# Optimization experiments

Hardware: AMD Instinct MI355X
Metric: run time of the kernel (lower is better)

## Reference

```python
import jax, jax.numpy as jnp
import numpy as np

LN_EPS = 1e-5


def setup_inputs() -> dict:
    key = jax.random.key(0)
    ks = jax.random.split(key, 6)
    B, M, N, D = 16, 128, 128, 128
    NM, H = 16, 512
    xav = float(np.sqrt(2.0 / (D + D)))  # xavier_normal over (in_dim, out_dim) fan
    return {
        "x": jax.random.normal(ks[0], (B, M, N, D), jnp.float32),
        "w1": jax.random.normal(ks[1], (D, D, NM, 2), jnp.float32) * xav,
        "w2": jax.random.normal(ks[2], (D, D, NM, 2), jnp.float32) * xav,
        "ff_w0": jax.random.normal(ks[3], (D, H), jnp.float32) * float(1.0 / np.sqrt(D)),
        "ff_b0": jnp.zeros((H,), jnp.float32),
        "ff_w1": jax.random.normal(ks[4], (H, D), jnp.float32) * float(1.0 / np.sqrt(H)),
        "ff_b1": jnp.zeros((D,), jnp.float32),
        "ln_g": jnp.ones((D,), jnp.float32),
        "ln_b": jnp.zeros((D,), jnp.float32),
    }


def _layer_norm(h, g, b):
    mu = jnp.mean(h, axis=-1, keepdims=True)
    var = jnp.mean(jnp.square(h - mu), axis=-1, keepdims=True)
    return (h - mu) * jax.lax.rsqrt(var + LN_EPS) * g + b


def _forward_fourier(x, w1, w2):
    # x: [B, M, N, I] -> [B, I, M, N]
    xt = jnp.transpose(x, (0, 3, 1, 2))
    B, I, M, N = xt.shape
    nm = w1.shape[2]
    cw1 = w1[..., 0] + 1j * w1[..., 1]  # [I, O, nm]
    cw2 = w2[..., 0] + 1j * w2[..., 1]
    O = cw1.shape[1]

    # Fourier along last axis (y)
    fty = jnp.fft.rfft(xt, axis=-1, norm="ortho")                    # [B,I,M,N//2+1]
    f1 = jnp.einsum("bixy,ioy->boxy", fty[..., :nm], cw1)            # [B,O,M,nm]
    pad_y = jnp.zeros((B, O, M, N // 2 + 1 - nm), dtype=f1.dtype)
    xy = jnp.fft.irfft(jnp.concatenate([f1, pad_y], axis=-1), n=N, axis=-1, norm="ortho")

    # Fourier along second-to-last axis (x)
    ftx = jnp.fft.rfft(xt, axis=-2, norm="ortho")                    # [B,I,M//2+1,N]
    f2 = jnp.einsum("bixy,iox->boxy", ftx[:, :, :nm, :], cw2)        # [B,O,nm,N]
    pad_x = jnp.zeros((B, O, M // 2 + 1 - nm, N), dtype=f2.dtype)
    xx = jnp.fft.irfft(jnp.concatenate([f2, pad_x], axis=-2), n=M, axis=-2, norm="ortho")

    return jnp.transpose(xx + xy, (0, 2, 3, 1))  # [B,M,N,O]


def reference(x, w1, w2, ff_w0, ff_b0, ff_w1, ff_b1, ln_g, ln_b):
    h = _forward_fourier(x, w1, w2)
    # backcast FeedForward: Linear -> ReLU -> Linear -> LayerNorm (dropout=0)
    h1 = jax.nn.relu(jnp.einsum("bmni,ih->bmnh", h, ff_w0) + ff_b0)
    h2 = jnp.einsum("bmnh,ho->bmno", h1, ff_w1) + ff_b1
    return _layer_norm(h2, ln_g, ln_b)
```

## Files before the change

kernel.cpp:

```cpp
#include <hip/hip_runtime.h>


#define LN_EPS 1e-5f
#define NMODES 16
#define FROW 4096
#define HROW 16384

typedef __attribute__((ext_vector_type(8))) short short8;
typedef __attribute__((ext_vector_type(8))) ushort ushort8;
typedef __attribute__((ext_vector_type(4))) short short4v;
typedef __attribute__((ext_vector_type(4))) float f32x4;

__device__ __forceinline__ ushort f2bf(float f) {
    unsigned u = __float_as_uint(f);
    unsigned r = (u + 0x7FFFu + ((u >> 16) & 1u)) >> 16;
    return (ushort)r;
}
__device__ __forceinline__ float bf2f(ushort h) {
    return __uint_as_float(((unsigned)h) << 16);
}

__global__ void k_setup(float* __restrict__ Tc, float* __restrict__ Ts,
                        float* __restrict__ IT) {
    const float invs = 0.08838834764831845f;
    for (int idx = threadIdx.x; idx < NMODES * 128; idx += blockDim.x) {
        int k = idx >> 7, n = idx & 127;
        int p = (k * n) & 127;
        float th = (float)p * (6.283185307179586f / 128.0f);
        float c = cosf(th), s = sinf(th);
        Tc[idx] = c * invs;
        Ts[idx] = -s * invs;
        float ck = (k == 0) ? invs : 2.0f * invs;
        IT[n * 32 + 2 * k]     = ck * c;
        IT[n * 32 + 2 * k + 1] = -ck * s;
    }
}

__global__ void k_wpack(const float* __restrict__ w, ushort* __restrict__ Wph,
                        ushort* __restrict__ Wpl) {
    int idx = blockIdx.x * 256 + threadIdx.x;
    int k  = idx >> 16;
    int op = (idx >> 8) & 255;
    int ip = idx & 255;
    int i = ip & 127, o = op & 127;
    const float* base = w + (((i << 7) | o) * NMODES + k) * 2;
    float re = base[0], im = base[1];
    float v = (ip < 128) ? ((op < 128) ? re : im)
                         : ((op < 128) ? -im : re);
    ushort hi = f2bf(v);
    ushort lo = f2bf(v - bf2f(hi));
    Wph[idx] = hi;
    Wpl[idx] = lo;
}

__global__ __launch_bounds__(256) void k_wcvt(const float* __restrict__ w0,
        const float* __restrict__ w1, ushort* __restrict__ w0t,
        ushort* __restrict__ w1t) {
    int idx = blockIdx.x * 256 + threadIdx.x;
    int h = idx >> 7, k = idx & 127;
    w0t[idx] = f2bf(w0[k * 512 + h]);
    int o = idx >> 9, hh = idx & 511;
    w1t[idx] = f2bf(w1[hh * 128 + o]);
}

__global__ __launch_bounds__(128) void k_fft(const float* __restrict__ x,
        const float* __restrict__ Tc, const float* __restrict__ Ts,
        float* __restrict__ F, int mode) {
    __shared__ float Tc_s[NMODES * 128];
    __shared__ float Ts_s[NMODES * 128];
    for (int e = threadIdx.x; e < NMODES * 128; e += 128) {
        Tc_s[e] = Tc[e];
        Ts_s[e] = Ts[e];
    }
    __syncthreads();
    int row = blockIdx.x;
    int base, ts;
    if (mode == 0) { base = row * HROW; ts = 128; }
    else { base = (row >> 7) * 2097152 + (row & 127) * 128; ts = 16384; }
    int i = threadIdx.x;
    float re[NMODES], im[NMODES];
#pragma unroll
    for (int k = 0; k < NMODES; ++k) { re[k] = 0.f; im[k] = 0.f; }
    for (int tb = 0; tb < 32; ++tb) {
        int t0 = tb * 4;
        float xv0 = x[base + (t0 + 0) * ts + i];
        float xv1 = x[base + (t0 + 1) * ts + i];
        float xv2 = x[base + (t0 + 2) * ts + i];
        float xv3 = x[base + (t0 + 3) * ts + i];
#pragma unroll
        for (int k = 0; k < NMODES; ++k) {
            f32x4 c4 = *(const f32x4*)&Tc_s[k * 128 + t0];
            f32x4 s4 = *(const f32x4*)&Ts_s[k * 128 + t0];
            re[k] += xv0 * c4[0] + xv1 * c4[1] + xv2 * c4[2] + xv3 * c4[3];
            im[k] += xv0 * s4[0] + xv1 * s4[1] + xv2 * s4[2] + xv3 * s4[3];
        }
    }
    float* outp = F + row * FROW;
#pragma unroll
    for (int k = 0; k < NMODES; ++k) {
        outp[k * 256 + i]       = re[k];
        outp[k * 256 + 128 + i] = im[k];
    }
}

__global__ __launch_bounds__(256) void k_mixm(const float* __restrict__ A,
        const ushort* __restrict__ Wph, const ushort* __restrict__ Wpl,
        float* __restrict__ outF) {
    __shared__ ushort Ah[32 * 264];
    __shared__ ushort Al[32 * 264];
    int tid = threadIdx.x;
    int kt = blockIdx.x & 15;
    int bm0 = (blockIdx.x >> 4) * 32;
    {
        int row = tid >> 3, cg = tid & 7;
        const float* arow = A + (bm0 + row) * FROW + kt * 256 + cg * 32;
        ushort* ah = &Ah[row * 264 + cg * 32];
        ushort* al = &Al[row * 264 + cg * 32];
#pragma unroll
        for (int j = 0; j < 8; ++j) {
            f32x4 v = *(const f32x4*)(arow + j * 4);
            short4v h4, l4;
#pragma unroll
            for (int q = 0; q < 4; ++q) {
                ushort h = f2bf(v[q]);
                h4[q] = (short)h;
                l4[q] = (short)f2bf(v[q] - bf2f(h));
            }
            *(short4v*)(ah + j * 4) = h4;
            *(short4v*)(al + j * 4) = l4;
        }
    }
    __syncthreads();
    int lane = tid & 63, wid = tid >> 6;
    int frow = lane & 15, fk8 = (lane >> 4) * 8, fr4 = (lane >> 4) * 4;
    f32x4 acc[2][4];
#pragma unroll
    for (int a = 0; a < 2; ++a)
#pragma unroll
        for (int c = 0; c < 4; ++c) acc[a][c] = {0.f, 0.f, 0.f, 0.f};
    const ushort* wph = Wph + kt * 65536;
    const ushort* wpl = Wpl + kt * 65536;
#pragma unroll
    for (int kk = 0; kk < 8; ++kk) {
        short8 ah0 = *(const short8*)&Ah[(frow)      * 264 + kk * 32 + fk8];
        short8 ah1 = *(const short8*)&Ah[(16 + frow) * 264 + kk * 32 + fk8];
        short8 al0 = *(const short8*)&Al[(frow)      * 264 + kk * 32 + fk8];
        short8 al1 = *(const short8*)&Al[(16 + frow) * 264 + kk * 32 + fk8];
#pragma unroll
        for (int tc = 0; tc < 4; ++tc) {
            int op = wid * 64 + tc * 16 + frow;
            int base = op * 256 + kk * 32 + fk8;
            short8 wh = *(const short8*)&wph[base];
            short8 wl = *(const short8*)&wpl[base];
            acc[0][tc] = __builtin_amdgcn_mfma_f32_16x16x32_bf16(ah0, wh, acc[0][tc], 0, 0, 0);
            acc[0][tc] = __builtin_amdgcn_mfma_f32_16x16x32_bf16(ah0, wl, acc[0][tc], 0, 0, 0);
            acc[0][tc] = __builtin_amdgcn_mfma_f32_16x16x32_bf16(al0, wh, acc[0][tc], 0, 0, 0);
            acc[1][tc] = __builtin_amdgcn_mfma_f32_16x16x32_bf16(ah1, wh, acc[1][tc], 0, 0, 0);
            acc[1][tc] = __builtin_amdgcn_mfma_f32_16x16x32_bf16(ah1, wl, acc[1][tc], 0, 0, 0);
            acc[1][tc] = __builtin_amdgcn_mfma_f32_16x16x32_bf16(al1, wh, acc[1][tc], 0, 0, 0);
        }
    }
#pragma unroll
    for (int tr = 0; tr < 2; ++tr)
#pragma unroll
        for (int tc = 0; tc < 4; ++tc)
#pragma unroll
            for (int r = 0; r < 4; ++r)
                outF[(bm0 + tr * 16 + fr4 + r) * FROW + kt * 256 + wid * 64 + tc * 16 + frow]
                    = acc[tr][tc][r];
}

__global__ __launch_bounds__(256) void k_icdft(const float* __restrict__ f,
        const float* __restrict__ IT, ushort* __restrict__ obf,
        float* __restrict__ h32, ushort* __restrict__ hbfs, int mode) {
    __shared__ float IT_s[128 * 32];
    __shared__ float f_s[32 * 128];
    int row = blockIdx.x;
    for (int e = threadIdx.x; e < 4096; e += 256) {
        IT_s[e] = IT[e];
        f_s[e]  = f[row * FROW + e];
    }
    __syncthreads();
    int o = threadIdx.x & 127, nh = threadIdx.x >> 7;
    for (int nb = 0; nb < 8; ++nb) {
        int n0 = nh * 64 + nb * 8;
        float acc[8];
#pragma unroll
        for (int j = 0; j < 8; ++j) acc[j] = 0.f;
#pragma unroll
        for (int kpb = 0; kpb < 8; ++kpb) {
            int kp0 = kpb * 4;
            float f0 = f_s[kp0 * 128 + o];
            float f1v = f_s[kp0 * 128 + 128 + o];
            float f2v = f_s[kp0 * 128 + 256 + o];
            float f3v = f_s[kp0 * 128 + 384 + o];
#pragma unroll
            for (int j = 0; j < 8; ++j) {
                f32x4 it = *(const f32x4*)&IT_s[(n0 + j) * 32 + kp0];
                acc[j] += f0 * it[0] + f1v * it[1] + f2v * it[2] + f3v * it[3];
            }
        }
        if (mode == 0) {
#pragma unroll
            for (int j = 0; j < 8; ++j)
                obf[row * HROW + (n0 + j) * 128 + o] = f2bf(acc[j]);
        } else if (mode == 1) {
#pragma unroll
            for (int j = 0; j < 8; ++j)
                h32[row * HROW + (n0 + j) * 128 + o] = acc[j];
        } else {
#pragma unroll
            for (int j = 0; j < 8; ++j) {
                int ix = (row >> 7) * 2097152 + (row & 127) * 128 + o + (n0 + j) * 16384;
                hbfs[ix] = f2bf(h32[ix] + acc[j]);
            }
        }
    }
}

__global__ __launch_bounds__(64, 2) void k_ffn(const ushort* __restrict__ hy,
        const ushort* __restrict__ hx, const ushort* __restrict__ hbfs,
        float* __restrict__ out,
        const ushort* __restrict__ w0t, const float* __restrict__ b0,
        const ushort* __restrict__ w1t, const float* __restrict__ b1,
        const float* __restrict__ g, const float* __restrict__ bb, int two) {
    __shared__ __align__(16) ushort h_s[64 * 136];
    __shared__ __align__(16) ushort h1_s[64 * 40];
    int lane = threadIdx.x;
    int R0 = blockIdx.x * 64;

    if (two) {
        int b = R0 >> 14, m = (R0 >> 7) & 127, n0 = R0 & 127;
        const ushort* hyp = hy + (size_t)R0 * 128;
        const ushort* hxp = hx + (size_t)b * 2097152 + (size_t)n0 * 16384 + m * 128;
        for (int e = lane; e < 1024; e += 64) {
            int rl = e >> 4, c8 = (e & 15) * 8;
            ushort8 a = *(const ushort8*)&hyp[rl * 128 + c8];
            ushort8 c = *(const ushort8*)&hxp[rl * 16384 + c8];
            ushort8 t;
#pragma unroll
            for (int j = 0; j < 8; ++j) t[j] = f2bf(bf2f(a[j]) + bf2f(c[j]));
            *(ushort8*)&h_s[rl * 136 + c8] = t;
        }
    } else {
        for (int e = lane; e < 1024; e += 64) {
            int rl = e >> 4, c8 = (e & 15) * 8;
            *(ushort8*)&h_s[rl * 136 + c8] =
                *(const ushort8*)&hbfs[(size_t)(R0 + rl) * 128 + c8];
        }
    }
    __syncthreads();

    int frow = lane & 15, qg = lane >> 4;
    int fk8 = qg * 8, fr4 = qg * 4;

    f32x4 acc2[4][8];
#pragma unroll
    for (int a = 0; a < 4; ++a)
#pragma unroll
        for (int c = 0; c < 8; ++c) acc2[a][c] = {0.f, 0.f, 0.f, 0.f};

    for (int ch = 0; ch < 16; ++ch) {
        short8 bfr[2][4];
#pragma unroll
        for (int tc2 = 0; tc2 < 2; ++tc2)
#pragma unroll
            for (int kk = 0; kk < 4; ++kk)
                bfr[tc2][kk] = *(const short8*)&w0t[(ch * 32 + tc2 * 16 + frow) * 128 + kk * 32 + fk8];
        f32x4 acc1[4][2];
#pragma unroll
        for (int a = 0; a < 4; ++a)
#pragma unroll
            for (int c = 0; c < 2; ++c) acc1[a][c] = {0.f, 0.f, 0.f, 0.f};
#pragma unroll
        for (int kk = 0; kk < 4; ++kk)
#pragma unroll
            for (int tr = 0; tr < 4; ++tr) {
                short8 av = *(const short8*)&h_s[(tr * 16 + frow) * 136 + kk * 32 + fk8];
#pragma unroll
                for (int tc2 = 0; tc2 < 2; ++tc2)
                    acc1[tr][tc2] = __builtin_amdgcn_mfma_f32_16x16x32_bf16(
                        av, bfr[tc2][kk], acc1[tr][tc2], 0, 0, 0);
            }
#pragma unroll
        for (int tc2 = 0; tc2 < 2; ++tc2) {
            float b0v = b0[ch * 32 + tc2 * 16 + frow];
#pragma unroll
            for (int tr = 0; tr < 4; ++tr)
#pragma unroll
                for (int r = 0; r < 4; ++r)
                    h1_s[(tr * 16 + fr4 + r) * 40 + tc2 * 16 + frow] =
                        f2bf(fmaxf(acc1[tr][tc2][r] + b0v, 0.f));
        }
        short8 b2[8];
#pragma unroll
        for (int tc = 0; tc < 8; ++tc)
            b2[tc] = *(const short8*)&w1t[(tc * 16 + frow) * 512 + ch * 32 + fk8];
#pragma unroll
        for (int tr = 0; tr < 4; ++tr) {
            short8 a2 = *(const short8*)&h1_s[(tr * 16 + frow) * 40 + fk8];
#pragma unroll
            for (int tc = 0; tc < 8; ++tc)
                acc2[tr][tc] = __builtin_amdgcn_mfma_f32_16x16x32_bf16(
                    a2, b2[tc], acc2[tr][tc], 0, 0, 0);
        }
    }

    float b1v[8], gv[8], bv[8];
#pragma unroll
    for (int tc = 0; tc < 8; ++tc) {
        int o = tc * 16 + frow;
        b1v[tc] = b1[o]; gv[tc] = g[o]; bv[tc] = bb[o];
    }
#pragma unroll
    for (int tr = 0; tr < 4; ++tr)
#pragma unroll
        for (int r = 0; r < 4; ++r) {
            float s = 0.f, qq = 0.f;
#pragma unroll
            for (int tc = 0; tc < 8; ++tc) {
                float v = acc2[tr][tc][r] + b1v[tc];
                acc2[tr][tc][r] = v;
                s += v; qq += v * v;
            }
            s += __shfl_xor(s, 1); qq += __shfl_xor(qq, 1);
            s += __shfl_xor(s, 2); qq += __shfl_xor(qq, 2);
            s += __shfl_xor(s, 4); qq += __shfl_xor(qq, 4);
            s += __shfl_xor(s, 8); qq += __shfl_xor(qq, 8);
            float mu = s * (1.0f / 128.0f);
            float var = qq * (1.0f / 128.0f) - mu * mu;
            float rs = rsqrtf(fmaxf(var, 0.f) + LN_EPS);
            float* orow = &out[(size_t)(R0 + tr * 16 + fr4 + r) * 128];
#pragma unroll
            for (int tc = 0; tc < 8; ++tc)
                orow[tc * 16 + frow] = (acc2[tr][tc][r] - mu) * rs * gv[tc] + bv[tc];
        }
}

extern "C" void kernel_launch(void* const* d_in, const int* in_sizes, int n_in,
                              void* d_out, int out_size, void* d_ws, size_t ws_size,
                              hipStream_t stream) {
    (void)in_sizes; (void)n_in; (void)out_size;
    const float* x   = (const float*)d_in[0];
    const float* w1  = (const float*)d_in[1];
    const float* w2  = (const float*)d_in[2];
    const float* fw0 = (const float*)d_in[3];
    const float* fb0 = (const float*)d_in[4];
    const float* fw1 = (const float*)d_in[5];
    const float* fb1 = (const float*)d_in[6];
    const float* lng = (const float*)d_in[7];
    const float* lnb = (const float*)d_in[8];
    float* out = (float*)d_out;

    char* ws = (char*)d_ws;
    float*  Tc  = (float*)(ws);
    float*  Ts  = (float*)(ws + 8192);
    float*  IT  = (float*)(ws + 16384);
    ushort* Wph = (ushort*)(ws + 32768);
    ushort* Wpl = (ushort*)(ws + 32768 + 2097152);
    ushort* w0t = (ushort*)(ws + 4227072);
    ushort* w1t = (ushort*)(ws + 4358144);
    float*  buf0 = (float*)(ws + 4489216);
    ushort* hy   = (ushort*)(ws + 38043648);
    ushort* hx   = (ushort*)(ws + 105152512);
    const size_t need_two = 172261376ull;
    int two = (ws_size >= need_two) ? 1 : 0;
    ushort* hbfs = hy;

    k_setup<<<1, 256, 0, stream>>>(Tc, Ts, IT);
    k_wcvt <<<256, 256, 0, stream>>>(fw0, fw1, w0t, w1t);

    k_wpack<<<4096, 256, 0, stream>>>(w1, Wph, Wpl);
    k_fft  <<<2048, 128, 0, stream>>>(x, Tc, Ts, buf0, 0);
    k_mixm <<<1024, 256, 0, stream>>>(buf0, Wph, Wpl, buf0);
    if (two) k_icdft<<<2048, 256, 0, stream>>>(buf0, IT, hy, out, hbfs, 0);
    else     k_icdft<<<2048, 256, 0, stream>>>(buf0, IT, hy, out, hbfs, 1);

    k_wpack<<<4096, 256, 0, stream>>>(w2, Wph, Wpl);
    k_fft  <<<2048, 128, 0, stream>>>(x, Tc, Ts, buf0, 1);
    k_mixm <<<1024, 256, 0, stream>>>(buf0, Wph, Wpl, buf0);
    if (two) k_icdft<<<2048, 256, 0, stream>>>(buf0, IT, hx, out, hbfs, 0);
    else     k_icdft<<<2048, 256, 0, stream>>>(buf0, IT, hx, out, hbfs, 2);

    k_ffn<<<4096, 64, 0, stream>>>(hy, hx, hbfs, out, w0t, fb0, w1t, fb1, lng, lnb, two);
}
```

Baseline: 522.5 us.

## Prefetch FFN weights, batch staging loads, split acc1 and change LDS padding

In the FFN kernel, the next chunk's W0 fragments are now loaded while the current chunk's second GEMM runs. The first GEMM is split into two row groups so fewer accumulators are live, and the chunk loop is kept rolled. The staging of hy+hx into shared memory now issues eight global vector loads before doing any conversion, to expose more memory-level parallelism. LDS row strides change from 136/40 to 134/38 to alter the bank mapping, but those rows are no longer 16-byte aligned for the ushort8/short8 accesses. That can split or slow the vector LDS operations.

New measurement: 604.3 us. 15.6% more time.

```diff
diff --git a/kernel.cpp b/kernel.cpp
--- a/kernel.cpp
+++ b/kernel.cpp
@@ -224,8 +224,8 @@
         const ushort* __restrict__ w0t, const float* __restrict__ b0,
         const ushort* __restrict__ w1t, const float* __restrict__ b1,
         const float* __restrict__ g, const float* __restrict__ bb, int two) {
-    __shared__ __align__(16) ushort h_s[64 * 136];
-    __shared__ __align__(16) ushort h1_s[64 * 40];
+    __shared__ __align__(16) ushort h_s[64 * 134];
+    __shared__ __align__(16) ushort h1_s[64 * 38];
     int lane = threadIdx.x;
     int R0 = blockIdx.x * 64;
 
@@ -233,19 +233,32 @@
         int b = R0 >> 14, m = (R0 >> 7) & 127, n0 = R0 & 127;
         const ushort* hyp = hy + (size_t)R0 * 128;
         const ushort* hxp = hx + (size_t)b * 2097152 + (size_t)n0 * 16384 + m * 128;
-        for (int e = lane; e < 1024; e += 64) {
+#pragma unroll
+        for (int half = 0; half < 2; ++half) {
+            ushort8 ay[8], ax[8];
+#pragma unroll
+            for (int i = 0; i < 8; ++i) {
+                int e = lane + (half * 8 + i) * 64;
+                int rl = e >> 4, c8 = (e & 15) * 8;
+                ay[i] = *(const ushort8*)&hyp[rl * 128 + c8];
+                ax[i] = *(const ushort8*)&hxp[rl * 16384 + c8];
+            }
+#pragma unroll
+            for (int i = 0; i < 8; ++i) {
+                int e = lane + (half * 8 + i) * 64;
+                int rl = e >> 4, c8 = (e & 15) * 8;
+                ushort8 t;
+#pragma unroll
+                for (int j = 0; j < 8; ++j) t[j] = f2bf(bf2f(ay[i][j]) + bf2f(ax[i][j]));
+                *(ushort8*)&h_s[rl * 134 + c8] = t;
+            }
+        }
+    } else {
+#pragma unroll
+        for (int i = 0; i < 16; ++i) {
+            int e = lane + i * 64;
             int rl = e >> 4, c8 = (e & 15) * 8;
-            ushort8 a = *(const ushort8*)&hyp[rl * 128 + c8];
-            ushort8 c = *(const ushort8*)&hxp[rl * 16384 + c8];
-            ushort8 t;
-#pragma unroll
-            for (int j = 0; j < 8; ++j) t[j] = f2bf(bf2f(a[j]) + bf2f(c[j]));
-            *(ushort8*)&h_s[rl * 136 + c8] = t;
-        }
-    } else {
-        for (int e = lane; e < 1024; e += 64) {
-            int rl = e >> 4, c8 = (e & 15) * 8;
-            *(ushort8*)&h_s[rl * 136 + c8] =
+            *(ushort8*)&h_s[rl * 134 + c8] =
                 *(const ushort8*)&hbfs[(size_t)(R0 + rl) * 128 + c8];
         }
     }
@@ -260,45 +273,64 @@
 #pragma unroll
         for (int c = 0; c < 8; ++c) acc2[a][c] = {0.f, 0.f, 0.f, 0.f};
 
+    short8 bfr[2][4];
+#pragma unroll
+    for (int tc2 = 0; tc2 < 2; ++tc2)
+#pragma unroll
+        for (int kk = 0; kk < 4; ++kk)
+            bfr[tc2][kk] = *(const short8*)&w0t[(tc2 * 16 + frow) * 128 + kk * 32 + fk8];
+
+#pragma unroll 1
     for (int ch = 0; ch < 16; ++ch) {
-        short8 bfr[2][4];
-#pragma unroll
-        for (int tc2 = 0; tc2 < 2; ++tc2)
-#pragma unroll
-            for (int kk = 0; kk < 4; ++kk)
-                bfr[tc2][kk] = *(const short8*)&w0t[(ch * 32 + tc2 * 16 + frow) * 128 + kk * 32 + fk8];
-        f32x4 acc1[4][2];
-#pragma unroll
-        for (int a = 0; a < 4; ++a)
-#pragma unroll
-            for (int c = 0; c < 2; ++c) acc1[a][c] = {0.f, 0.f, 0.f, 0.f};
-#pragma unroll
-        for (int kk = 0; kk < 4; ++kk)
-#pragma unroll
-            for (int tr = 0; tr < 4; ++tr) {
-                short8 av = *(const short8*)&h_s[(tr * 16 + frow) * 136 + kk * 32 + fk8];
-#pragma unroll
-                for (int tc2 = 0; tc2 < 2; ++tc2)
-                    acc1[tr][tc2] = __builtin_amdgcn_mfma_f32_16x16x32_bf16(
-                        av, bfr[tc2][kk], acc1[tr][tc2], 0, 0, 0);
-            }
-#pragma unroll
-        for (int tc2 = 0; tc2 < 2; ++tc2) {
-            float b0v = b0[ch * 32 + tc2 * 16 + frow];
-#pragma unroll
-            for (int tr = 0; tr < 4; ++tr)
-#pragma unroll
-                for (int r = 0; r < 4; ++r)
-                    h1_s[(tr * 16 + fr4 + r) * 40 + tc2 * 16 + frow] =
-                        f2bf(fmaxf(acc1[tr][tc2][r] + b0v, 0.f));
-        }
         short8 b2[8];
 #pragma unroll
         for (int tc = 0; tc < 8; ++tc)
             b2[tc] = *(const short8*)&w1t[(tc * 16 + frow) * 512 + ch * 32 + fk8];
+        float b0v0 = b0[ch * 32 + frow];
+        float b0v1 = b0[ch * 32 + 16 + frow];
+
+#pragma unroll
+        for (int g2 = 0; g2 < 2; ++g2) {
+            f32x4 acc1[2][2];
+#pragma unroll
+            for (int a = 0; a < 2; ++a)
+#pragma unroll
+                for (int c = 0; c < 2; ++c) acc1[a][c] = {0.f, 0.f, 0.f, 0.f};
+#pragma unroll
+            for (int kk = 0; kk < 4; ++kk)
+#pragma unroll
+                for (int t2 = 0; t2 < 2; ++t2) {
+                    int tr = g2 * 2 + t2;
+                    short8 av = *(const short8*)&h_s[(tr * 16 + frow) * 134 + kk * 32 + fk8];
+                    acc1[t2][0] = __builtin_amdgcn_mfma_f32_16x16x32_bf16(
+                        av, bfr[0][kk], acc1[t2][0], 0, 0, 0);
+                    acc1[t2][1] = __builtin_amdgcn_mfma_f32_16x16x32_bf16(
+                        av, bfr[1][kk], acc1[t2][1], 0, 0, 0);
+                }
+#pragma unroll
+            for (int t2 = 0; t2 < 2; ++t2)
+#pragma unroll
+                for (int r = 0; r < 4; ++r) {
+                    int rowl = (g2 * 2 + t2) * 16 + fr4 + r;
+                    h1_s[rowl * 38 + frow] =
+                        f2bf(fmaxf(acc1[t2][0][r] + b0v0, 0.f));
+                    h1_s[rowl * 38 + 16 + frow] =
+                        f2bf(fmaxf(acc1[t2][1][r] + b0v1, 0.f));
+                }
+        }
+
+        if (ch < 15) {
+#pragma unroll
+            for (int tc2 = 0; tc2 < 2; ++tc2)
+#pragma unroll
+                for (int kk = 0; kk < 4; ++kk)
+                    bfr[tc2][kk] = *(const short8*)
+                        &w0t[((ch + 1) * 32 + tc2 * 16 + frow) * 128 + kk * 32 + fk8];
+        }
+
 #pragma unroll
         for (int tr = 0; tr < 4; ++tr) {
-            short8 a2 = *(const short8*)&h1_s[(tr * 16 + frow) * 40 + fk8];
+            short8 a2 = *(const short8*)&h1_s[(tr * 16 + frow) * 38 + fk8];
 #pragma unroll
             for (int tc = 0; tc < 8; ++tc)
                 acc2[tr][tc] = __builtin_amdgcn_mfma_f32_16x16x32_bf16(
```
